# Kernel tuning notes

Measured on AMD Instinct MI355X. Metric: run time of the kernel, lower is better.

The kernel has to match this reference:

```python
import jax, jax.numpy as jnp
import numpy as np

LORA_RANK = 16
LORA_ALPHA = 32.0
LORA_SCALE = LORA_ALPHA / LORA_RANK
W_BITS = 8
A_BITS = 8


def fake_quant(x, bits):
    """Symmetric per-tensor fake quantization with straight-through estimator."""
    qmax = 2.0 ** (bits - 1) - 1.0
    scale = jnp.maximum(jnp.max(jnp.abs(x)), 1e-8) / qmax
    q = jnp.clip(jnp.round(x / scale), -qmax, qmax) * scale
    return x + jax.lax.stop_gradient(q - x)  # STE


def quant_linear_lora(x, W, b, A, B):
    # x: [..., in], W: [out, in], A: [r, in], B: [out, r]
    xq = fake_quant(x, A_BITS)
    Wq = fake_quant(W, W_BITS)
    base = jnp.einsum('bsi,oi->bso', xq, Wq) + b
    lora = jnp.einsum('bsr,or->bso', jnp.einsum('bsi,ri->bsr', x, A), B)
    return base + LORA_SCALE * lora


def setup_inputs() -> dict:
    key = jax.random.key(0)
    ks = jax.random.split(key, 9)
    n_embd, d_ff, B_, S = 1024, 4096, 4, 2048
    s_in = 1.0 / np.sqrt(n_embd)
    s_ff = 1.0 / np.sqrt(d_ff)
    return {
        'hidden_states': jax.random.normal(ks[0], (B_, S, n_embd), jnp.float32),
        'W_fc': jax.random.normal(ks[1], (d_ff, n_embd), jnp.float32) * s_in,
        'b_fc': jax.random.normal(ks[2], (d_ff,), jnp.float32) * 0.02,
        'A_fc': jax.random.normal(ks[3], (LORA_RANK, n_embd), jnp.float32) * s_in,
        'B_fc': jax.random.normal(ks[4], (d_ff, LORA_RANK), jnp.float32) * 0.01,
        'W_proj': jax.random.normal(ks[5], (n_embd, d_ff), jnp.float32) * s_ff,
        'b_proj': jax.random.normal(ks[6], (n_embd,), jnp.float32) * 0.02,
        'A_proj': jax.random.normal(ks[7], (LORA_RANK, d_ff), jnp.float32) * s_ff,
        'B_proj': jax.random.normal(ks[8], (n_embd, LORA_RANK), jnp.float32) * 0.01,
    }


def reference(hidden_states, W_fc, b_fc, A_fc, B_fc, W_proj, b_proj, A_proj, B_proj):
    h = quant_linear_lora(hidden_states, W_fc, b_fc, A_fc, B_fc)
    h = jax.nn.gelu(h, approximate=False)  # nn.GELU() default = exact erf GELU
    h = quant_linear_lora(h, W_proj, b_proj, A_proj, B_proj)
    return h
```

## Files before the change

kernel.cpp:

```cpp
#include <hip/hip_runtime.h>
#include <stdint.h>

using i32x4 = __attribute__((ext_vector_type(4))) int;
using f32x4 = __attribute__((ext_vector_type(4))) float;
using f16x4 = __attribute__((ext_vector_type(4))) _Float16;

#define M_TOK 8192
#define N_EMB 1024
#define D_FF  4096

__device__ __forceinline__ void async_lds16(void* lds, const void* g) {
  __builtin_amdgcn_global_load_lds(
      (const __attribute__((address_space(1))) void*)g,
      (__attribute__((address_space(3))) void*)lds, 16, 0, 0);
}

__global__ void zero_slots_k(unsigned* s) {
  if (threadIdx.x < 16) s[threadIdx.x] = 0u;
}

__global__ void absmax_k(const float* __restrict__ p, long n, unsigned* __restrict__ slot) {
  long i = ((long)blockIdx.x * blockDim.x + threadIdx.x) * 4;
  long stride = (long)gridDim.x * blockDim.x * 4;
  float m = 0.f;
  for (; i < n; i += stride) {
    float4 v = *(const float4*)(p + i);
    m = fmaxf(m, fmaxf(fmaxf(fabsf(v.x), fabsf(v.y)), fmaxf(fabsf(v.z), fabsf(v.w))));
  }
  for (int o = 32; o; o >>= 1) m = fmaxf(m, __shfl_xor(m, o));
  __shared__ float sm[4];
  if ((threadIdx.x & 63) == 0) sm[threadIdx.x >> 6] = m;
  __syncthreads();
  if (threadIdx.x == 0) {
    m = fmaxf(fmaxf(sm[0], sm[1]), fmaxf(sm[2], sm[3]));
    atomicMax(slot, __float_as_uint(m));
  }
}

__global__ void quant_k(const float* __restrict__ p, int8_t* __restrict__ q, long n,
                        const unsigned* __restrict__ slot) {
  float inv = 127.f / fmaxf(__uint_as_float(*slot), 1e-8f);
  long i = ((long)blockIdx.x * blockDim.x + threadIdx.x) * 4;
  long stride = (long)gridDim.x * blockDim.x * 4;
  for (; i < n; i += stride) {
    float4 v = *(const float4*)(p + i);
    int b0 = (int)fminf(fmaxf(rintf(v.x * inv), -127.f), 127.f);
    int b1 = (int)fminf(fmaxf(rintf(v.y * inv), -127.f), 127.f);
    int b2 = (int)fminf(fmaxf(rintf(v.z * inv), -127.f), 127.f);
    int b3 = (int)fminf(fmaxf(rintf(v.w * inv), -127.f), 127.f);
    int w = (b0 & 0xff) | ((b1 & 0xff) << 8) | ((b2 & 0xff) << 16) | ((b3 & 0xff) << 24);
    *(int*)(q + i) = w;
  }
}

__global__ void prep_bfrag_k(const float* __restrict__ A, _Float16* __restrict__ Bp, int K) {
  int s = blockIdx.x;
  int l = threadIdx.x;
  int r = l & 15, g = l >> 4;
  float4 v = *(const float4*)(A + (long)r * K + s * 16 + g * 4);
  f16x4 h;
  h[0] = (_Float16)v.x; h[1] = (_Float16)v.y; h[2] = (_Float16)v.z; h[3] = (_Float16)v.w;
  *(f16x4*)(Bp + ((long)s * 64 + l) * 4) = h;
}

__global__ __launch_bounds__(512) void lora_quant_k(
    const float* __restrict__ X, const _Float16* __restrict__ Bpre,
    const unsigned* __restrict__ slot, int8_t* __restrict__ Q,
    float* __restrict__ T, int K) {
  int lane = threadIdx.x & 63, wave = threadIdx.x >> 6;
  int row0 = blockIdx.x * 16;
  int r = lane & 15, g = lane >> 4;
  float inv = 127.f / fmaxf(__uint_as_float(*slot), 1e-8f);

  int kPerWave = K >> 3;
  int kbase = wave * kPerWave;
  const float* xrow = X + (long)(row0 + r) * K;
  int8_t* qrow = Q + (long)(row0 + r) * K;

  f32x4 acc = {0.f, 0.f, 0.f, 0.f};
  int nsteps = kPerWave >> 4;
#pragma unroll 4
  for (int s = 0; s < nsteps; s++) {
    int k = kbase + s * 16 + g * 4;
    float4 v = *(const float4*)(xrow + k);
    int b0 = (int)fminf(fmaxf(rintf(v.x * inv), -127.f), 127.f);
    int b1 = (int)fminf(fmaxf(rintf(v.y * inv), -127.f), 127.f);
    int b2 = (int)fminf(fmaxf(rintf(v.z * inv), -127.f), 127.f);
    int b3 = (int)fminf(fmaxf(rintf(v.w * inv), -127.f), 127.f);
    *(int*)(qrow + k) = (b0 & 0xff) | ((b1 & 0xff) << 8) | ((b2 & 0xff) << 16) | ((b3 & 0xff) << 24);
    f16x4 a;
    a[0] = (_Float16)v.x; a[1] = (_Float16)v.y; a[2] = (_Float16)v.z; a[3] = (_Float16)v.w;
    int gs = (kbase + s * 16) >> 4;
    f16x4 b = *(const f16x4*)(Bpre + ((long)gs * 64 + lane) * 4);
    acc = __builtin_amdgcn_mfma_f32_16x16x16f16(a, b, acc, 0, 0, 0);
  }

  __shared__ float part[8][16][17];
#pragma unroll
  for (int j = 0; j < 4; j++) part[wave][g * 4 + j][r] = acc[j];
  __syncthreads();
  int t = threadIdx.x;
  if (t < 256) {
    int m = t >> 4, rr = t & 15;
    float sum = 0.f;
#pragma unroll
    for (int w = 0; w < 8; w++) sum += part[w][m][rr];
    T[(long)(row0 + m) * 16 + rr] = 2.0f * sum;
  }
}

template <bool GELU>
__global__ __launch_bounds__(256, 2) void gemm_q8(
    const int8_t* __restrict__ Aq, const int8_t* __restrict__ Bq,
    int M, int N, int K,
    const unsigned* __restrict__ sa, const unsigned* __restrict__ sb,
    const float* __restrict__ bias,
    const float* __restrict__ T,
    const float* __restrict__ Bl,
    float* __restrict__ C, unsigned* hmax) {
  __shared__ __align__(16) int8_t As[8192];
  __shared__ __align__(16) int8_t Bs[8192];

  int nwg = gridDim.x * gridDim.y;
  int lid = blockIdx.y * gridDim.x + blockIdx.x;
  int q8 = nwg >> 3;
  int nid = (lid & 7) * q8 + (lid >> 3);
  int bn = (nid % gridDim.x) * 128;
  int bm = (nid / gridDim.x) * 128;

  int t = threadIdx.x;
  int lane = t & 63, wave = t >> 6;
  int wr = wave >> 1, wc = wave & 1;
  int l16 = lane & 15, lq = lane >> 4;

  int a0 = t * 16, a1 = (256 + t) * 16;
  int kq0 = a0 >> 11, row0 = (a0 >> 4) & 127;
  int kq1 = a1 >> 11, row1 = (a1 >> 4) & 127;

  const int8_t* Abase = Aq + (long)bm * K;
  const int8_t* Bbase = Bq + (long)bn * K;
  const int8_t* srcA0 = Abase + (long)row0 * K + kq0 * 16;
  const int8_t* srcA1 = Abase + (long)row1 * K + kq1 * 16;
  const int8_t* srcB0 = Bbase + (long)row0 * K + kq0 * 16;
  const int8_t* srcB1 = Bbase + (long)row1 * K + kq1 * 16;

  i32x4 acc[4][4] = {};

  int KT = K >> 6;
  for (int kt = 0; kt < KT; kt++) {
    long koff = (long)kt * 64;
    async_lds16(As + a0, srcA0 + koff);
    async_lds16(As + a1, srcA1 + koff);
    async_lds16(Bs + a0, srcB0 + koff);
    async_lds16(Bs + a1, srcB1 + koff);
    __syncthreads();

    i32x4 av[4], bv[4];
#pragma unroll
    for (int mf = 0; mf < 4; mf++)
      av[mf] = *(const i32x4*)(As + lq * 2048 + (wr * 64 + mf * 16 + l16) * 16);
#pragma unroll
    for (int nf = 0; nf < 4; nf++)
      bv[nf] = *(const i32x4*)(Bs + lq * 2048 + (wc * 64 + nf * 16 + l16) * 16);
#pragma unroll
    for (int mf = 0; mf < 4; mf++)
#pragma unroll
      for (int nf = 0; nf < 4; nf++)
        acc[mf][nf] = __builtin_amdgcn_mfma_i32_16x16x64_i8(av[mf], bv[nf], acc[mf][nf], 0, 0, 0);
    __syncthreads();
  }

  float s = (fmaxf(__uint_as_float(*sa), 1e-8f) * (1.f / 127.f)) *
            (fmaxf(__uint_as_float(*sb), 1e-8f) * (1.f / 127.f));

  f16x4 af[4], bf[4];
#pragma unroll
  for (int mf = 0; mf < 4; mf++) {
    int m = bm + wr * 64 + mf * 16 + l16;
    float4 tv = *(const float4*)(T + (long)m * 16 + lq * 4);
    f16x4 v; v[0] = (_Float16)tv.x; v[1] = (_Float16)tv.y; v[2] = (_Float16)tv.z; v[3] = (_Float16)tv.w;
    af[mf] = v;
  }
#pragma unroll
  for (int nf = 0; nf < 4; nf++) {
    int n = bn + wc * 64 + nf * 16 + l16;
    float4 bv4 = *(const float4*)(Bl + (long)n * 16 + lq * 4);
    f16x4 v; v[0] = (_Float16)bv4.x; v[1] = (_Float16)bv4.y; v[2] = (_Float16)bv4.z; v[3] = (_Float16)bv4.w;
    bf[nf] = v;
  }
  float bias_v[4];
#pragma unroll
  for (int nf = 0; nf < 4; nf++) bias_v[nf] = bias[bn + wc * 64 + nf * 16 + l16];

  float lmax = 0.f;
#pragma unroll
  for (int mf = 0; mf < 4; mf++) {
#pragma unroll
    for (int nf = 0; nf < 4; nf++) {
      f32x4 fa = __builtin_amdgcn_mfma_f32_16x16x16f16(af[mf], bf[nf], f32x4{0.f, 0.f, 0.f, 0.f}, 0, 0, 0);
      int n = bn + wc * 64 + nf * 16 + l16;
#pragma unroll
      for (int j = 0; j < 4; j++) {
        int m = bm + wr * 64 + mf * 16 + lq * 4 + j;
        float v = s * (float)acc[mf][nf][j] + bias_v[nf] + fa[j];
        if constexpr (GELU) {
          v = 0.5f * v * (1.0f + erff(v * 0.70710678118654752f));
          lmax = fmaxf(lmax, fabsf(v));
        }
        C[(long)m * N + n] = v;
      }
    }
  }
  if constexpr (GELU) {
    for (int o = 32; o; o >>= 1) lmax = fmaxf(lmax, __shfl_xor(lmax, o));
    if (lane == 0) atomicMax(hmax, __float_as_uint(lmax));
  }
}

extern "C" void kernel_launch(void* const* d_in, const int* in_sizes, int n_in,
                              void* d_out, int out_size, void* d_ws, size_t ws_size,
                              hipStream_t stream) {
  const float* x   = (const float*)d_in[0];
  const float* Wfc = (const float*)d_in[1];
  const float* bfc = (const float*)d_in[2];
  const float* Afc = (const float*)d_in[3];
  const float* Bfc = (const float*)d_in[4];
  const float* Wpj = (const float*)d_in[5];
  const float* bpj = (const float*)d_in[6];
  const float* Apj = (const float*)d_in[7];
  const float* Bpj = (const float*)d_in[8];
  float* out = (float*)d_out;

  char* ws = (char*)d_ws;
  unsigned* slots = (unsigned*)ws;
  int8_t* qx  = (int8_t*)(ws + 256);
  int8_t* qwf = qx  + (size_t)M_TOK * N_EMB;
  int8_t* qwp = qwf + (size_t)D_FF * N_EMB;
  int8_t* qh  = qwp + (size_t)N_EMB * D_FF;
  float*  t1  = (float*)(qh + (size_t)M_TOK * D_FF);
  float*  t2  = t1  + (size_t)M_TOK * 16;
  _Float16* Bp1 = (_Float16*)(t2 + (size_t)M_TOK * 16);
  _Float16* Bp2 = Bp1 + (size_t)N_EMB * 16;
  float*  h   = (float*)(Bp2 + (size_t)D_FF * 16);

  zero_slots_k<<<1, 64, 0, stream>>>(slots);
  absmax_k<<<1024, 256, 0, stream>>>(x,   (long)M_TOK * N_EMB, slots + 0);
  absmax_k<<<1024, 256, 0, stream>>>(Wfc, (long)D_FF * N_EMB,  slots + 1);
  absmax_k<<<1024, 256, 0, stream>>>(Wpj, (long)N_EMB * D_FF,  slots + 2);

  quant_k<<<2048, 256, 0, stream>>>(Wfc, qwf, (long)D_FF * N_EMB, slots + 1);
  quant_k<<<2048, 256, 0, stream>>>(Wpj, qwp, (long)N_EMB * D_FF, slots + 2);

  prep_bfrag_k<<<N_EMB / 16, 64, 0, stream>>>(Afc, Bp1, N_EMB);
  prep_bfrag_k<<<D_FF / 16, 64, 0, stream>>>(Apj, Bp2, D_FF);

  lora_quant_k<<<M_TOK / 16, 512, 0, stream>>>(x, Bp1, slots + 0, qx, t1, N_EMB);

  gemm_q8<true><<<dim3(D_FF / 128, M_TOK / 128), 256, 0, stream>>>(
      qx, qwf, M_TOK, D_FF, N_EMB, slots + 0, slots + 1, bfc, t1, Bfc, h, slots + 3);

  lora_quant_k<<<M_TOK / 16, 512, 0, stream>>>(h, Bp2, slots + 3, qh, t2, D_FF);

  gemm_q8<false><<<dim3(N_EMB / 128, M_TOK / 128), 256, 0, stream>>>(
      qh, qwp, M_TOK, N_EMB, D_FF, slots + 3, slots + 2, bpj, t2, Bpj, out, nullptr);
}
```

Baseline: 338.0 us.

## Double-buffer int8 GEMM LDS tiles with BK=128 and XOR-swizzled layout

Reworks the int8 GEMM main loop to prefetch the next 128-wide K tile into a second LDS buffer while MFMAs run on the current one, cutting one barrier per iteration. LDS tiles become row-major with XOR swizzling of 16-byte column groups to avoid bank conflicts, and s_setprio is raised around the MFMA block. LDS use grows to 64KB per block, which may limit occupancy below the two blocks per CU the launch bounds request.

```diff
diff --git a/kernel.cpp b/kernel.cpp
--- a/kernel.cpp
+++ b/kernel.cpp
@@ -118,8 +118,7 @@
     const float* __restrict__ T,
     const float* __restrict__ Bl,
     float* __restrict__ C, unsigned* hmax) {
-  __shared__ __align__(16) int8_t As[8192];
-  __shared__ __align__(16) int8_t Bs[8192];
+  __shared__ __align__(16) int8_t lds[65536];
 
   int nwg = gridDim.x * gridDim.y;
   int lid = blockIdx.y * gridDim.x + blockIdx.x;
@@ -133,41 +132,84 @@
   int wr = wave >> 1, wc = wave & 1;
   int l16 = lane & 15, lq = lane >> 4;
 
-  int a0 = t * 16, a1 = (256 + t) * 16;
-  int kq0 = a0 >> 11, row0 = (a0 >> 4) & 127;
-  int kq1 = a1 >> 11, row1 = (a1 >> 4) & 127;
-
-  const int8_t* Abase = Aq + (long)bm * K;
-  const int8_t* Bbase = Bq + (long)bn * K;
-  const int8_t* srcA0 = Abase + (long)row0 * K + kq0 * 16;
-  const int8_t* srcA1 = Abase + (long)row1 * K + kq1 * 16;
-  const int8_t* srcB0 = Bbase + (long)row0 * K + kq0 * 16;
-  const int8_t* srcB1 = Bbase + (long)row1 * K + kq1 * 16;
+  int ldst[4];
+  const int8_t* srcA[4];
+  const int8_t* srcB[4];
+#pragma unroll
+  for (int i = 0; i < 4; i++) {
+    int s = i * 256 + t;
+    int row = s >> 3;
+    int cg = (t & 7) ^ (row & 7);
+    ldst[i] = s * 16;
+    srcA[i] = Aq + (long)(bm + row) * K + cg * 16;
+    srcB[i] = Bq + (long)(bn + row) * K + cg * 16;
+  }
+
+  int aoff[4][2], boff[4][2];
+#pragma unroll
+  for (int mf = 0; mf < 4; mf++) {
+    int row = wr * 64 + mf * 16 + l16;
+#pragma unroll
+    for (int kh = 0; kh < 2; kh++) {
+      int c = kh * 4 + lq;
+      aoff[mf][kh] = row * 128 + ((c ^ (row & 7)) << 4);
+    }
+  }
+#pragma unroll
+  for (int nf = 0; nf < 4; nf++) {
+    int row = wc * 64 + nf * 16 + l16;
+#pragma unroll
+    for (int kh = 0; kh < 2; kh++) {
+      int c = kh * 4 + lq;
+      boff[nf][kh] = row * 128 + ((c ^ (row & 7)) << 4);
+    }
+  }
 
   i32x4 acc[4][4] = {};
-
-  int KT = K >> 6;
+  int KT = K >> 7;
+
+  {
+#pragma unroll
+    for (int i = 0; i < 4; i++) {
+      async_lds16(lds + ldst[i], srcA[i]);
+      async_lds16(lds + 16384 + ldst[i], srcB[i]);
+    }
+  }
+  __syncthreads();
+
+  int cur = 0;
   for (int kt = 0; kt < KT; kt++) {
-    long koff = (long)kt * 64;
-    async_lds16(As + a0, srcA0 + koff);
-    async_lds16(As + a1, srcA1 + koff);
-    async_lds16(Bs + a0, srcB0 + koff);
-    async_lds16(Bs + a1, srcB1 + koff);
+    if (kt + 1 < KT) {
+      long ko = (long)(kt + 1) * 128;
+      const int8_t* A_l_next_dummy;
+      (void)A_l_next_dummy;
+      int nb = (cur ^ 1) * 32768;
+#pragma unroll
+      for (int i = 0; i < 4; i++) {
+        async_lds16(lds + nb + ldst[i], srcA[i] + ko);
+        async_lds16(lds + nb + 16384 + ldst[i], srcB[i] + ko);
+      }
+    }
+
+    const int8_t* A_l = lds + cur * 32768;
+    const int8_t* B_l = A_l + 16384;
+#pragma unroll
+    for (int kh = 0; kh < 2; kh++) {
+      i32x4 av[4], bv[4];
+#pragma unroll
+      for (int mf = 0; mf < 4; mf++) av[mf] = *(const i32x4*)(A_l + aoff[mf][kh]);
+#pragma unroll
+      for (int nf = 0; nf < 4; nf++) bv[nf] = *(const i32x4*)(B_l + boff[nf][kh]);
+      __builtin_amdgcn_s_setprio(1);
+#pragma unroll
+      for (int mf = 0; mf < 4; mf++)
+#pragma unroll
+        for (int nf = 0; nf < 4; nf++)
+          acc[mf][nf] = __builtin_amdgcn_mfma_i32_16x16x64_i8(av[mf], bv[nf], acc[mf][nf], 0, 0, 0);
+      __builtin_amdgcn_s_setprio(0);
+    }
     __syncthreads();
-
-    i32x4 av[4], bv[4];
-#pragma unroll
-    for (int mf = 0; mf < 4; mf++)
-      av[mf] = *(const i32x4*)(As + lq * 2048 + (wr * 64 + mf * 16 + l16) * 16);
-#pragma unroll
-    for (int nf = 0; nf < 4; nf++)
-      bv[nf] = *(const i32x4*)(Bs + lq * 2048 + (wc * 64 + nf * 16 + l16) * 16);
-#pragma unroll
-    for (int mf = 0; mf < 4; mf++)
-#pragma unroll
-      for (int nf = 0; nf < 4; nf++)
-        acc[mf][nf] = __builtin_amdgcn_mfma_i32_16x16x64_i8(av[mf], bv[nf], acc[mf][nf], 0, 0, 0);
-    __syncthreads();
+    cur ^= 1;
   }
 
   float s = (fmaxf(__uint_as_float(*sa), 1e-8f) * (1.f / 127.f)) *
```

Result: faster. 305.9 us (-9.5%).

## Triple-buffer int8 GEMM LDS loads and widen tile to 128x256 with 8 waves

Applied to the files above, without the earlier changes.

The int8 GEMM now uses a 128x256 output tile with 512 threads (8 waves in a 2x4 grid) and a three-stage LDS ring. Async global-to-LDS loads run two K-steps ahead, and a partial vmcnt wait plus a single barrier replaces the old load/sync/compute/sync pattern. MFMA sections are wrapped in setprio, and the LDS layout changes to row-major 64-byte rows. This aims to hide global load latency and raise operand reuse. The costs are 72KB of LDS per block, which limits occupancy, and possible LDS bank conflicts from the new layout.

```diff
diff --git a/kernel.cpp b/kernel.cpp
--- a/kernel.cpp
+++ b/kernel.cpp
@@ -110,7 +110,7 @@
 }
 
 template <bool GELU>
-__global__ __launch_bounds__(256, 2) void gemm_q8(
+__global__ __launch_bounds__(512, 4) void gemm_q8(
     const int8_t* __restrict__ Aq, const int8_t* __restrict__ Bq,
     int M, int N, int K,
     const unsigned* __restrict__ sa, const unsigned* __restrict__ sb,
@@ -118,56 +118,77 @@
     const float* __restrict__ T,
     const float* __restrict__ Bl,
     float* __restrict__ C, unsigned* hmax) {
-  __shared__ __align__(16) int8_t As[8192];
-  __shared__ __align__(16) int8_t Bs[8192];
+  __shared__ __align__(16) int8_t sm[73728];
 
   int nwg = gridDim.x * gridDim.y;
   int lid = blockIdx.y * gridDim.x + blockIdx.x;
   int q8 = nwg >> 3;
   int nid = (lid & 7) * q8 + (lid >> 3);
-  int bn = (nid % gridDim.x) * 128;
+  int bn = (nid % gridDim.x) * 256;
   int bm = (nid / gridDim.x) * 128;
 
   int t = threadIdx.x;
   int lane = t & 63, wave = t >> 6;
-  int wr = wave >> 1, wc = wave & 1;
+  int wr = wave >> 2, wc = wave & 3;
   int l16 = lane & 15, lq = lane >> 4;
 
-  int a0 = t * 16, a1 = (256 + t) * 16;
-  int kq0 = a0 >> 11, row0 = (a0 >> 4) & 127;
-  int kq1 = a1 >> 11, row1 = (a1 >> 4) & 127;
-
-  const int8_t* Abase = Aq + (long)bm * K;
-  const int8_t* Bbase = Bq + (long)bn * K;
-  const int8_t* srcA0 = Abase + (long)row0 * K + kq0 * 16;
-  const int8_t* srcA1 = Abase + (long)row1 * K + kq1 * 16;
-  const int8_t* srcB0 = Bbase + (long)row0 * K + kq0 * 16;
-  const int8_t* srcB1 = Bbase + (long)row1 * K + kq1 * 16;
+  const int8_t* srcA0 = Aq + (long)(bm + (t >> 2)) * K + (t & 3) * 16;
+  const int8_t* srcB0 = Bq + (long)(bn + (t >> 2)) * K + (t & 3) * 16;
+  const int8_t* srcB1 = Bq + (long)(bn + ((512 + t) >> 2)) * K + (t & 3) * 16;
+  int dA = t * 16;
+  int dB0 = t * 16;
+  int dB1 = 8192 + t * 16;
+
+  int aoff[4], boff[4];
+#pragma unroll
+  for (int mf = 0; mf < 4; mf++) aoff[mf] = (wr * 64 + mf * 16 + l16) * 64 + lq * 16;
+#pragma unroll
+  for (int nf = 0; nf < 4; nf++) boff[nf] = (wc * 64 + nf * 16 + l16) * 64 + lq * 16;
 
   i32x4 acc[4][4] = {};
-
   int KT = K >> 6;
-  for (int kt = 0; kt < KT; kt++) {
-    long koff = (long)kt * 64;
-    async_lds16(As + a0, srcA0 + koff);
-    async_lds16(As + a1, srcA1 + koff);
-    async_lds16(Bs + a0, srcB0 + koff);
-    async_lds16(Bs + a1, srcB1 + koff);
-    __syncthreads();
+
+  async_lds16(sm + dA, srcA0);
+  async_lds16(sm + 8192 + dB0, srcB0);
+  async_lds16(sm + 8192 + dB1, srcB1);
+  async_lds16(sm + 24576 + dA, srcA0 + 64);
+  async_lds16(sm + 24576 + 8192 + dB0, srcB0 + 64);
+  async_lds16(sm + 24576 + 8192 + dB1, srcB1 + 64);
+  __syncthreads();
+
+  for (int kt = 0; kt < KT; ++kt) {
+    const int8_t* base = sm + (kt % 3) * 24576;
+    if (kt + 2 < KT) {
+      int8_t* nb = sm + ((kt + 2) % 3) * 24576;
+      long ko = (long)(kt + 2) * 64;
+      async_lds16(nb + dA, srcA0 + ko);
+      async_lds16(nb + 8192 + dB0, srcB0 + ko);
+      async_lds16(nb + 8192 + dB1, srcB1 + ko);
+    }
 
     i32x4 av[4], bv[4];
 #pragma unroll
-    for (int mf = 0; mf < 4; mf++)
-      av[mf] = *(const i32x4*)(As + lq * 2048 + (wr * 64 + mf * 16 + l16) * 16);
-#pragma unroll
-    for (int nf = 0; nf < 4; nf++)
-      bv[nf] = *(const i32x4*)(Bs + lq * 2048 + (wc * 64 + nf * 16 + l16) * 16);
+    for (int nf = 0; nf < 4; nf++) bv[nf] = *(const i32x4*)(base + 8192 + boff[nf]);
+#pragma unroll
+    for (int mf = 0; mf < 4; mf++) av[mf] = *(const i32x4*)(base + aoff[mf]);
+
+    __builtin_amdgcn_s_setprio(1);
 #pragma unroll
     for (int mf = 0; mf < 4; mf++)
 #pragma unroll
       for (int nf = 0; nf < 4; nf++)
         acc[mf][nf] = __builtin_amdgcn_mfma_i32_16x16x64_i8(av[mf], bv[nf], acc[mf][nf], 0, 0, 0);
-    __syncthreads();
+    __builtin_amdgcn_s_setprio(0);
+
+    if (kt + 1 < KT) {
+      if (kt + 2 < KT) {
+        asm volatile("s_waitcnt vmcnt(3)" ::: "memory");
+      } else {
+        asm volatile("s_waitcnt vmcnt(0)" ::: "memory");
+      }
+      __builtin_amdgcn_s_barrier();
+      __builtin_amdgcn_sched_barrier(0);
+    }
   }
 
   float s = (fmaxf(__uint_as_float(*sa), 1e-8f) * (1.f / 127.f)) *
@@ -256,11 +277,11 @@
 
   lora_quant_k<<<M_TOK / 16, 512, 0, stream>>>(x, Bp1, slots + 0, qx, t1, N_EMB);
 
-  gemm_q8<true><<<dim3(D_FF / 128, M_TOK / 128), 256, 0, stream>>>(
+  gemm_q8<true><<<dim3(D_FF / 256, M_TOK / 128), 512, 0, stream>>>(
       qx, qwf, M_TOK, D_FF, N_EMB, slots + 0, slots + 1, bfc, t1, Bfc, h, slots + 3);
 
   lora_quant_k<<<M_TOK / 16, 512, 0, stream>>>(h, Bp2, slots + 3, qh, t2, D_FF);
 
-  gemm_q8<false><<<dim3(N_EMB / 128, M_TOK / 128), 256, 0, stream>>>(
+  gemm_q8<false><<<dim3(N_EMB / 256, M_TOK / 128), 512, 0, stream>>>(
       qh, qwp, M_TOK, N_EMB, D_FF, slots + 3, slots + 2, bpj, t2, Bpj, out, nullptr);
 }
```

Result: faster. 301.6 us (-10.8%).

## Pre-pack int8 operands into MFMA fragment order and drop LDS staging in GEMM

Applied to the files above, without the earlier changes.

Weights and activations are quantized straight into a tiled layout where each 16x64 tile is stored in the exact per-lane order the i8 MFMA expects. The GEMM then reads fragments directly from global memory into registers, with no LDS staging and no barriers, using a 256x64 block tile with 8x2 fragments per wave. The absmax and weight-quant launches are also merged into fewer kernels. The trade-off is that operand reuse now depends on caches rather than LDS, and the larger per-wave accumulator raises register pressure.

```diff
diff --git a/kernel.cpp b/kernel.cpp
--- a/kernel.cpp
+++ b/kernel.cpp
@@ -9,17 +9,18 @@
 #define N_EMB 1024
 #define D_FF  4096
 
-__device__ __forceinline__ void async_lds16(void* lds, const void* g) {
-  __builtin_amdgcn_global_load_lds(
-      (const __attribute__((address_space(1))) void*)g,
-      (__attribute__((address_space(3))) void*)lds, 16, 0, 0);
-}
-
 __global__ void zero_slots_k(unsigned* s) {
   if (threadIdx.x < 16) s[threadIdx.x] = 0u;
 }
 
-__global__ void absmax_k(const float* __restrict__ p, long n, unsigned* __restrict__ slot) {
+__global__ void absmax3_k(const float* __restrict__ p0, long n0,
+                          const float* __restrict__ p1, long n1,
+                          const float* __restrict__ p2, long n2,
+                          unsigned* __restrict__ slots) {
+  const float* p = blockIdx.y == 0 ? p0 : (blockIdx.y == 1 ? p1 : p2);
+  long n = blockIdx.y == 0 ? n0 : (blockIdx.y == 1 ? n1 : n2);
+  unsigned* slot = slots + blockIdx.y;
+
   long i = ((long)blockIdx.x * blockDim.x + threadIdx.x) * 4;
   long stride = (long)gridDim.x * blockDim.x * 4;
   float m = 0.f;
@@ -37,20 +38,32 @@
   }
 }
 
-__global__ void quant_k(const float* __restrict__ p, int8_t* __restrict__ q, long n,
-                        const unsigned* __restrict__ slot) {
-  float inv = 127.f / fmaxf(__uint_as_float(*slot), 1e-8f);
-  long i = ((long)blockIdx.x * blockDim.x + threadIdx.x) * 4;
-  long stride = (long)gridDim.x * blockDim.x * 4;
-  for (; i < n; i += stride) {
-    float4 v = *(const float4*)(p + i);
+__global__ void wquant_pack2_k(const float* __restrict__ W0, int8_t* __restrict__ P0, int K0,
+                               const float* __restrict__ W1, int8_t* __restrict__ P1, int K1,
+                               const unsigned* __restrict__ slots) {
+  const float* W = blockIdx.y ? W1 : W0;
+  int8_t* P = blockIdx.y ? P1 : P0;
+  int K = blockIdx.y ? K1 : K0;
+  float inv = 127.f / fmaxf(__uint_as_float(slots[blockIdx.y + 1]), 1e-8f);
+
+  int tile = blockIdx.x * 4 + (threadIdx.x >> 6);
+  int lane = threadIdx.x & 63;
+  int KT = K >> 6;
+  int mt = tile / KT, kt = tile % KT;
+  const float* src = W + (long)(mt * 16 + (lane & 15)) * K + kt * 64 + (lane >> 4) * 16;
+
+  int words[4];
+#pragma unroll
+  for (int j = 0; j < 4; j++) {
+    float4 v = *(const float4*)(src + j * 4);
     int b0 = (int)fminf(fmaxf(rintf(v.x * inv), -127.f), 127.f);
     int b1 = (int)fminf(fmaxf(rintf(v.y * inv), -127.f), 127.f);
     int b2 = (int)fminf(fmaxf(rintf(v.z * inv), -127.f), 127.f);
     int b3 = (int)fminf(fmaxf(rintf(v.w * inv), -127.f), 127.f);
-    int w = (b0 & 0xff) | ((b1 & 0xff) << 8) | ((b2 & 0xff) << 16) | ((b3 & 0xff) << 24);
-    *(int*)(q + i) = w;
-  }
+    words[j] = (b0 & 0xff) | ((b1 & 0xff) << 8) | ((b2 & 0xff) << 16) | ((b3 & 0xff) << 24);
+  }
+  i32x4 out; out[0] = words[0]; out[1] = words[1]; out[2] = words[2]; out[3] = words[3];
+  *(i32x4*)(P + (long)tile * 1024 + lane * 16) = out;
 }
 
 __global__ void prep_bfrag_k(const float* __restrict__ A, _Float16* __restrict__ Bp, int K) {
@@ -69,25 +82,28 @@
     float* __restrict__ T, int K) {
   int lane = threadIdx.x & 63, wave = threadIdx.x >> 6;
   int row0 = blockIdx.x * 16;
-  int r = lane & 15, g = lane >> 4;
+  int r = lane & 15, g = threadIdx.x >> 4;
   float inv = 127.f / fmaxf(__uint_as_float(*slot), 1e-8f);
 
   int kPerWave = K >> 3;
   int kbase = wave * kPerWave;
   const float* xrow = X + (long)(row0 + r) * K;
-  int8_t* qrow = Q + (long)(row0 + r) * K;
-
+  int8_t* qtile = Q + (long)blockIdx.x * (K >> 6) * 1024;
+
+  int gl = lane >> 4;
   f32x4 acc = {0.f, 0.f, 0.f, 0.f};
   int nsteps = kPerWave >> 4;
 #pragma unroll 4
   for (int s = 0; s < nsteps; s++) {
-    int k = kbase + s * 16 + g * 4;
+    int k = kbase + s * 16 + gl * 4;
     float4 v = *(const float4*)(xrow + k);
     int b0 = (int)fminf(fmaxf(rintf(v.x * inv), -127.f), 127.f);
     int b1 = (int)fminf(fmaxf(rintf(v.y * inv), -127.f), 127.f);
     int b2 = (int)fminf(fmaxf(rintf(v.z * inv), -127.f), 127.f);
     int b3 = (int)fminf(fmaxf(rintf(v.w * inv), -127.f), 127.f);
-    *(int*)(qrow + k) = (b0 & 0xff) | ((b1 & 0xff) << 8) | ((b2 & 0xff) << 16) | ((b3 & 0xff) << 24);
+    int w = (b0 & 0xff) | ((b1 & 0xff) << 8) | ((b2 & 0xff) << 16) | ((b3 & 0xff) << 24);
+    long poff = (long)(k >> 6) * 1024 + ((r + (((k >> 4) & 3) << 4)) << 4) + (k & 15);
+    *(int*)(qtile + poff) = w;
     f16x4 a;
     a[0] = (_Float16)v.x; a[1] = (_Float16)v.y; a[2] = (_Float16)v.z; a[3] = (_Float16)v.w;
     int gs = (kbase + s * 16) >> 4;
@@ -97,7 +113,7 @@
 
   __shared__ float part[8][16][17];
 #pragma unroll
-  for (int j = 0; j < 4; j++) part[wave][g * 4 + j][r] = acc[j];
+  for (int j = 0; j < 4; j++) part[wave][gl * 4 + j][r] = acc[j];
   __syncthreads();
   int t = threadIdx.x;
   if (t < 256) {
@@ -110,98 +126,80 @@
 }
 
 template <bool GELU>
-__global__ __launch_bounds__(256, 2) void gemm_q8(
-    const int8_t* __restrict__ Aq, const int8_t* __restrict__ Bq,
-    int M, int N, int K,
+__global__ __launch_bounds__(256) void gemm_pk(
+    const int8_t* __restrict__ Apk, const int8_t* __restrict__ Bpk,
+    int N, int K,
     const unsigned* __restrict__ sa, const unsigned* __restrict__ sb,
     const float* __restrict__ bias,
     const float* __restrict__ T,
     const float* __restrict__ Bl,
     float* __restrict__ C, unsigned* hmax) {
-  __shared__ __align__(16) int8_t As[8192];
-  __shared__ __align__(16) int8_t Bs[8192];
-
   int nwg = gridDim.x * gridDim.y;
   int lid = blockIdx.y * gridDim.x + blockIdx.x;
-  int q8 = nwg >> 3;
-  int nid = (lid & 7) * q8 + (lid >> 3);
-  int bn = (nid % gridDim.x) * 128;
-  int bm = (nid / gridDim.x) * 128;
+  int cpx = nwg >> 3;
+  int nid = (lid & 7) * cpx + (lid >> 3);
+  int bn = (nid % gridDim.x) * 64;
+  int bm = (nid / gridDim.x) * 256;
 
   int t = threadIdx.x;
   int lane = t & 63, wave = t >> 6;
   int wr = wave >> 1, wc = wave & 1;
   int l16 = lane & 15, lq = lane >> 4;
 
-  int a0 = t * 16, a1 = (256 + t) * 16;
-  int kq0 = a0 >> 11, row0 = (a0 >> 4) & 127;
-  int kq1 = a1 >> 11, row1 = (a1 >> 4) & 127;
-
-  const int8_t* Abase = Aq + (long)bm * K;
-  const int8_t* Bbase = Bq + (long)bn * K;
-  const int8_t* srcA0 = Abase + (long)row0 * K + kq0 * 16;
-  const int8_t* srcA1 = Abase + (long)row1 * K + kq1 * 16;
-  const int8_t* srcB0 = Bbase + (long)row0 * K + kq0 * 16;
-  const int8_t* srcB1 = Bbase + (long)row1 * K + kq1 * 16;
-
-  i32x4 acc[4][4] = {};
-
   int KT = K >> 6;
-  for (int kt = 0; kt < KT; kt++) {
-    long koff = (long)kt * 64;
-    async_lds16(As + a0, srcA0 + koff);
-    async_lds16(As + a1, srcA1 + koff);
-    async_lds16(Bs + a0, srcB0 + koff);
-    async_lds16(Bs + a1, srcB1 + koff);
-    __syncthreads();
-
-    i32x4 av[4], bv[4];
-#pragma unroll
-    for (int mf = 0; mf < 4; mf++)
-      av[mf] = *(const i32x4*)(As + lq * 2048 + (wr * 64 + mf * 16 + l16) * 16);
-#pragma unroll
-    for (int nf = 0; nf < 4; nf++)
-      bv[nf] = *(const i32x4*)(Bs + lq * 2048 + (wc * 64 + nf * 16 + l16) * 16);
-#pragma unroll
-    for (int mf = 0; mf < 4; mf++)
-#pragma unroll
-      for (int nf = 0; nf < 4; nf++)
+  const int8_t* Ap = Apk + ((long)(bm >> 4) + wr * 8) * KT * 1024 + lane * 16;
+  const int8_t* Bp = Bpk + ((long)(bn >> 4) + wc * 2) * KT * 1024 + lane * 16;
+
+  i32x4 acc[8][2] = {};
+
+#pragma unroll 2
+  for (int kt = 0; kt < KT; ++kt) {
+    i32x4 av[8], bv[2];
+#pragma unroll
+    for (int mf = 0; mf < 8; mf++)
+      av[mf] = *(const i32x4*)(Ap + ((long)mf * KT + kt) * 1024);
+#pragma unroll
+    for (int nf = 0; nf < 2; nf++)
+      bv[nf] = *(const i32x4*)(Bp + ((long)nf * KT + kt) * 1024);
+#pragma unroll
+    for (int mf = 0; mf < 8; mf++)
+#pragma unroll
+      for (int nf = 0; nf < 2; nf++)
         acc[mf][nf] = __builtin_amdgcn_mfma_i32_16x16x64_i8(av[mf], bv[nf], acc[mf][nf], 0, 0, 0);
-    __syncthreads();
   }
 
   float s = (fmaxf(__uint_as_float(*sa), 1e-8f) * (1.f / 127.f)) *
             (fmaxf(__uint_as_float(*sb), 1e-8f) * (1.f / 127.f));
 
-  f16x4 af[4], bf[4];
-#pragma unroll
-  for (int mf = 0; mf < 4; mf++) {
-    int m = bm + wr * 64 + mf * 16 + l16;
+  f16x4 af[8], bf[2];
+#pragma unroll
+  for (int mf = 0; mf < 8; mf++) {
+    int m = bm + wr * 128 + mf * 16 + l16;
     float4 tv = *(const float4*)(T + (long)m * 16 + lq * 4);
     f16x4 v; v[0] = (_Float16)tv.x; v[1] = (_Float16)tv.y; v[2] = (_Float16)tv.z; v[3] = (_Float16)tv.w;
     af[mf] = v;
   }
 #pragma unroll
-  for (int nf = 0; nf < 4; nf++) {
-    int n = bn + wc * 64 + nf * 16 + l16;
+  for (int nf = 0; nf < 2; nf++) {
+    int n = bn + wc * 32 + nf * 16 + l16;
     float4 bv4 = *(const float4*)(Bl + (long)n * 16 + lq * 4);
     f16x4 v; v[0] = (_Float16)bv4.x; v[1] = (_Float16)bv4.y; v[2] = (_Float16)bv4.z; v[3] = (_Float16)bv4.w;
     bf[nf] = v;
   }
-  float bias_v[4];
-#pragma unroll
-  for (int nf = 0; nf < 4; nf++) bias_v[nf] = bias[bn + wc * 64 + nf * 16 + l16];
+  float bias_v[2];
+#pragma unroll
+  for (int nf = 0; nf < 2; nf++) bias_v[nf] = bias[bn + wc * 32 + nf * 16 + l16];
 
   float lmax = 0.f;
 #pragma unroll
-  for (int mf = 0; mf < 4; mf++) {
-#pragma unroll
-    for (int nf = 0; nf < 4; nf++) {
+  for (int mf = 0; mf < 8; mf++) {
+#pragma unroll
+    for (int nf = 0; nf < 2; nf++) {
       f32x4 fa = __builtin_amdgcn_mfma_f32_16x16x16f16(af[mf], bf[nf], f32x4{0.f, 0.f, 0.f, 0.f}, 0, 0, 0);
-      int n = bn + wc * 64 + nf * 16 + l16;
+      int n = bn + wc * 32 + nf * 16 + l16;
 #pragma unroll
       for (int j = 0; j < 4; j++) {
-        int m = bm + wr * 64 + mf * 16 + lq * 4 + j;
+        int m = bm + wr * 128 + mf * 16 + lq * 4 + j;
         float v = s * (float)acc[mf][nf][j] + bias_v[nf] + fa[j];
         if constexpr (GELU) {
           v = 0.5f * v * (1.0f + erff(v * 0.70710678118654752f));
@@ -244,23 +242,23 @@
   float*  h   = (float*)(Bp2 + (size_t)D_FF * 16);
 
   zero_slots_k<<<1, 64, 0, stream>>>(slots);
-  absmax_k<<<1024, 256, 0, stream>>>(x,   (long)M_TOK * N_EMB, slots + 0);
-  absmax_k<<<1024, 256, 0, stream>>>(Wfc, (long)D_FF * N_EMB,  slots + 1);
-  absmax_k<<<1024, 256, 0, stream>>>(Wpj, (long)N_EMB * D_FF,  slots + 2);
-
-  quant_k<<<2048, 256, 0, stream>>>(Wfc, qwf, (long)D_FF * N_EMB, slots + 1);
-  quant_k<<<2048, 256, 0, stream>>>(Wpj, qwp, (long)N_EMB * D_FF, slots + 2);
+
+  absmax3_k<<<dim3(1024, 3), 256, 0, stream>>>(
+      x, (long)M_TOK * N_EMB, Wfc, (long)D_FF * N_EMB, Wpj, (long)N_EMB * D_FF, slots);
+
+  wquant_pack2_k<<<dim3(1024, 2), 256, 0, stream>>>(
+      Wfc, qwf, N_EMB, Wpj, qwp, D_FF, slots);
 
   prep_bfrag_k<<<N_EMB / 16, 64, 0, stream>>>(Afc, Bp1, N_EMB);
   prep_bfrag_k<<<D_FF / 16, 64, 0, stream>>>(Apj, Bp2, D_FF);
 
   lora_quant_k<<<M_TOK / 16, 512, 0, stream>>>(x, Bp1, slots + 0, qx, t1, N_EMB);
 
-  gemm_q8<true><<<dim3(D_FF / 128, M_TOK / 128), 256, 0, stream>>>(
-      qx, qwf, M_TOK, D_FF, N_EMB, slots + 0, slots + 1, bfc, t1, Bfc, h, slots + 3);
+  gemm_pk<true><<<dim3(D_FF / 64, M_TOK / 256), 256, 0, stream>>>(
+      qx, qwf, D_FF, N_EMB, slots + 0, slots + 1, bfc, t1, Bfc, h, slots + 3);
 
   lora_quant_k<<<M_TOK / 16, 512, 0, stream>>>(h, Bp2, slots + 3, qh, t2, D_FF);
 
-  gemm_q8<false><<<dim3(N_EMB / 128, M_TOK / 128), 256, 0, stream>>>(
-      qh, qwp, M_TOK, N_EMB, D_FF, slots + 3, slots + 2, bpj, t2, Bpj, out, nullptr);
-}
+  gemm_pk<false><<<dim3(N_EMB / 64, M_TOK / 256), 256, 0, stream>>>(
+      qh, qwp, N_EMB, D_FF, slots + 3, slots + 2, bpj, t2, Bpj, out, nullptr);
+}
```

Result: faster. 285.6 us (-15.5%).
